# Optimization experiments

Measured on AMD Instinct MI355X. Metric: run time of the kernel, lower is better.

## Reference

```python
import jax, jax.numpy as jnp
import numpy as np

WIN = 12     # SAMv3 window_size
HEADS = 8    # num_heads

def _window(t, win=WIN):
    B, H, W, C = t.shape
    t = t.reshape(B, H // win, win, W // win, win, C).transpose(0, 1, 3, 2, 4, 5)
    return t.reshape(B, (H // win) * (W // win), win * win, C)

def _unwindow(t, H, W, win=WIN):
    B, nW, S, C = t.shape
    t = t.reshape(B, H // win, W // win, win, win, C).transpose(0, 1, 3, 2, 4, 5)
    return t.reshape(B, H, W, C)

def _sam(fq, fkv, bias, wq, wk, wv, wo, bo):
    # Windowed, masked cross-frame multi-head attention (SAMv3).
    # fq, fkv: (B, C, H, W); bias: (B, nW, 1, 1, S) additive mask bias.
    B, C, H, W = fq.shape
    hd = C // HEADS
    scale = hd ** -0.5
    q = _window(jnp.einsum('bchw,cd->bhwd', fq, wq))   # (B,nW,S,C)
    k = _window(jnp.einsum('bchw,cd->bhwd', fkv, wk))
    v = _window(jnp.einsum('bchw,cd->bhwd', fkv, wv))
    nW, S = q.shape[1], q.shape[2]
    q = q.reshape(B, nW, S, HEADS, hd)
    k = k.reshape(B, nW, S, HEADS, hd)
    v = v.reshape(B, nW, S, HEADS, hd)
    attn = jnp.einsum('bnqhd,bnkhd->bnhqk', q, k) * scale + bias
    attn = jax.nn.softmax(attn, axis=-1)
    out = jnp.einsum('bnhqk,bnkhd->bnqhd', attn, v).reshape(B, nW, S, C)
    out = out @ wo + bo
    return _unwindow(out, H, W).transpose(0, 3, 1, 2)  # (B, C, H, W)

def setup_inputs() -> dict:
    key = jax.random.key(0)
    B, C, T, H, W = 2, 384, 2, 192, 192
    ks = jax.random.split(key, 16)
    d = {}
    d['x'] = jax.random.normal(ks[0], (B, C, T, H, W), jnp.float32)
    d['mask'] = jax.random.randint(ks[1], (B, T, 1, H, W), 0, 2, jnp.int32)
    names = ['sam1_wq', 'sam1_wk', 'sam1_wv', 'sam1_wo',
             'sam2_wq', 'sam2_wk', 'sam2_wv', 'sam2_wo',
             'proj1_w', 'proj2_w']
    for i, n in enumerate(names):
        d[n] = jax.random.normal(ks[2 + i], (C, C), jnp.float32) * 0.02
    d['sam1_bo'] = jnp.zeros((C,), jnp.float32)
    d['sam2_bo'] = jnp.zeros((C,), jnp.float32)
    d['proj1_b'] = jnp.zeros((C,), jnp.float32)
    d['proj2_b'] = jnp.zeros((C,), jnp.float32)
    return d

def reference(x, mask, sam1_wq, sam1_wk, sam1_wv, sam1_wo, sam1_bo,
              sam2_wq, sam2_wk, sam2_wv, sam2_wo, sam2_bo,
              proj1_w, proj1_b, proj2_w, proj2_b):
    # x: (B, C, T=2, H, W); mask: (B, T, 1, H, W)
    f1 = x[:, :, 0]
    f2 = x[:, :, 1]
    m = mask[:, 1, 0][..., None]                      # (B, H, W, 1), frame-2 mask
    mw = _window(m)[..., 0]                           # (B, nW, S)
    bias = jnp.where(mw == 0, -1e9, 0.0).astype(x.dtype)[:, :, None, None, :]
    o1 = _sam(f1, f2, bias, sam1_wq, sam1_wk, sam1_wv, sam1_wo, sam1_bo)
    x1 = jnp.einsum('bchw,dc->bdhw', o1, proj1_w) + proj1_b[None, :, None, None]
    o2 = _sam(f2, f1, bias, sam2_wq, sam2_wk, sam2_wv, sam2_wo, sam2_bo)
    x2 = jnp.einsum('bchw,dc->bdhw', o2, proj2_w) + proj2_b[None, :, None, None]
    return jnp.concatenate([x1[:, :, None], x2[:, :, None]], axis=2)  # (B, C, 2, H, W)
```

## Files before the change

kernel.cpp:

```cpp
#include <hip/hip_runtime.h>
#include <stdint.h>

typedef __attribute__((ext_vector_type(8))) short bf16x8;
typedef __attribute__((ext_vector_type(4))) float f32x4;

#define HW    36864
#define CCH   384
#define NPIX  73728
#define W2    147456

__device__ __forceinline__ unsigned short f2bf(float f) {
  unsigned u = __builtin_bit_cast(unsigned, f);
  u += 0x7FFFu + ((u >> 16) & 1u);
  return (unsigned short)(u >> 16);
}

typedef const unsigned int __attribute__((address_space(1)))* gas1_t;
typedef unsigned int __attribute__((address_space(3)))* las3_t;
__device__ __forceinline__ void gload16(const void* g, void* l) {
  __builtin_amdgcn_global_load_lds((gas1_t)g, (las3_t)l, 16, 0, 0);
}


__global__ void k_wt(const float* __restrict__ w0, const float* __restrict__ w1,
                     const float* __restrict__ w2, const float* __restrict__ w3,
                     const float* __restrict__ w4, const float* __restrict__ w5,
                     unsigned short* __restrict__ wt) {
  int idx = blockIdx.x * 256 + threadIdx.x;
  int w = blockIdx.y;
  const float* W;
  switch (w) { case 0: W = w0; break; case 1: W = w1; break;
               case 2: W = w2; break; case 3: W = w3; break;
               case 4: W = w4; break; default: W = w5; break; }
  const int slotmap[6] = {0, 4, 5, 3, 1, 2};
  int slot = slotmap[w];
  int c = idx / 384, d = idx % 384;
  wt[(size_t)slot * W2 + (size_t)d * 384 + c] = f2bf(W[(size_t)c * 384 + d]);
}

__global__ void k_wf(const float* __restrict__ wo1, const float* __restrict__ pj1,
                     const float* __restrict__ wo2, const float* __restrict__ pj2,
                     unsigned short* __restrict__ wfT) {
  int idx = blockIdx.x * 256 + threadIdx.x;
  int s = blockIdx.y;
  const float* wo = s ? wo2 : wo1;
  const float* pj = s ? pj2 : pj1;
  int d = idx / 384, e = idx % 384;
  float acc = 0.f;
  for (int c = 0; c < 384; ++c) acc += pj[d * 384 + c] * wo[e * 384 + c];
  wfT[(size_t)s * W2 + (size_t)d * 384 + e] = f2bf(acc);
}

__global__ void k_bf(const float* __restrict__ bo1, const float* __restrict__ pj1,
                     const float* __restrict__ pb1, const float* __restrict__ bo2,
                     const float* __restrict__ pj2, const float* __restrict__ pb2,
                     float* __restrict__ bfused) {
  int t = threadIdx.x;
  int s = t / 384, d = t % 384;
  const float* bo = s ? bo2 : bo1;
  const float* pj = s ? pj2 : pj1;
  const float* pb = s ? pb2 : pb1;
  float acc = pb[d];
  for (int c = 0; c < 384; ++c) acc += pj[d * 384 + c] * bo[c];
  bfused[t] = acc;
}

__global__ __launch_bounds__(256) void k_tx(const float* __restrict__ x,
                                            unsigned short* __restrict__ xbf) {
  __shared__ float tile[64][65];
  int p0 = blockIdx.x * 64;
  int c0 = blockIdx.y * 64;
  int bt = blockIdx.z;
  int b = bt >> 1, t = bt & 1;
  int tid = threadIdx.x;
  int cl = tid >> 2;
  int pq = (tid & 3) * 4;
  const float* src = x + (((size_t)b * CCH + (c0 + cl)) * 2 + t) * HW + p0;
#pragma unroll
  for (int i = 0; i < 4; ++i) {
    int p_l = pq + i * 16;
    float4 v = *reinterpret_cast<const float4*>(src + p_l);
    tile[cl][p_l + 0] = v.x; tile[cl][p_l + 1] = v.y;
    tile[cl][p_l + 2] = v.z; tile[cl][p_l + 3] = v.w;
  }
  __syncthreads();
  int pl = tid >> 2;
  int cq = (tid & 3) * 16;
  unsigned short* dst = xbf + ((size_t)(t * 2 + b) * HW + p0 + pl) * CCH + c0 + cq;
  bf16x8 o0, o1;
#pragma unroll
  for (int j = 0; j < 8; ++j) o0[j] = (short)f2bf(tile[cq + j][pl]);
#pragma unroll
  for (int j = 0; j < 8; ++j) o1[j] = (short)f2bf(tile[cq + 8 + j][pl]);
  *reinterpret_cast<bf16x8*>(dst) = o0;
  *reinterpret_cast<bf16x8*>(dst + 8) = o1;
}

__global__ __launch_bounds__(256) void gemm_qkv(
    const unsigned short* __restrict__ A,
    const unsigned short* __restrict__ Bt,
    unsigned short* __restrict__ Cq,
    unsigned short* __restrict__ Ckv,
    float oscale) {
  __shared__ __align__(16) unsigned short Lsh[3][8192];
  const int tid = threadIdx.x;
  const int lane = tid & 63;
  const int wid = tid >> 6, wr = wid >> 1, wc = wid & 1;

  const int gx = gridDim.x;
  const int nwg = gx * gridDim.y;
  const int bid = blockIdx.x + blockIdx.y * gx;
  const int chunk = nwg >> 3;
  const int l = (bid & 7) * chunk + (bid >> 3);
  const int bx = l % gx, by = l / gx;

  const int m0 = by * 128;
  const int n0 = bx * 128;
  const int r15 = lane & 15, g = lane >> 4;

  const int u1 = tid + 256;
  const unsigned short* srcA0 = A + (size_t)(m0 + (tid >> 2)) * 384 + (((tid & 3) ^ ((tid >> 3) & 3)) << 3);
  const unsigned short* srcA1 = A + (size_t)(m0 + (u1 >> 2)) * 384 + (((u1 & 3) ^ ((u1 >> 3) & 3)) << 3);
  const unsigned short* srcB0 = Bt + (size_t)(n0 + (tid >> 2)) * 384 + (((tid & 3) ^ ((tid >> 3) & 3)) << 3);
  const unsigned short* srcB1 = Bt + (size_t)(n0 + (u1 >> 2)) * 384 + (((u1 & 3) ^ ((u1 >> 3) & 3)) << 3);
  const int wbase = (tid & ~63) * 8;

  f32x4 acc[4][4];
  f32x4 zero4 = {0.f, 0.f, 0.f, 0.f};
#pragma unroll
  for (int a = 0; a < 4; ++a)
#pragma unroll
    for (int b = 0; b < 4; ++b) acc[a][b] = zero4;

  const int swzr = (g ^ ((r15 >> 1) & 3)) << 3;

#define STAGE(buf, kt) do {                                  \
    int ke = (kt) * 32;                                      \
    gload16(srcA0 + ke, &Lsh[(buf)][wbase]);                 \
    gload16(srcA1 + ke, &Lsh[(buf)][2048 + wbase]);          \
    gload16(srcB0 + ke, &Lsh[(buf)][4096 + wbase]);          \
    gload16(srcB1 + ke, &Lsh[(buf)][6144 + wbase]);          \
  } while (0)

#define COMPUTE(buf) do {                                                       \
    bf16x8 af[4], bfv[4];                                                       \
    _Pragma("unroll")                                                           \
    for (int a = 0; a < 4; ++a)                                                 \
      af[a] = *(const bf16x8*)&Lsh[(buf)][(wr * 64 + a * 16 + r15) * 32 + swzr];\
    _Pragma("unroll")                                                           \
    for (int b = 0; b < 4; ++b)                                                 \
      bfv[b] = *(const bf16x8*)&Lsh[(buf)][4096 + (wc * 64 + b * 16 + r15) * 32 + swzr];\
    _Pragma("unroll")                                                           \
    for (int a = 0; a < 4; ++a)                                                 \
      _Pragma("unroll")                                                         \
      for (int b = 0; b < 4; ++b)                                               \
        acc[a][b] = __builtin_amdgcn_mfma_f32_16x16x32_bf16(af[a], bfv[b], acc[a][b], 0, 0, 0);\
  } while (0)

  STAGE(0, 0);
  STAGE(1, 1);
#pragma unroll
  for (int kt = 0; kt < 11; ++kt) {
    asm volatile("s_waitcnt vmcnt(4)" ::: "memory");
    __builtin_amdgcn_s_barrier();
    asm volatile("" ::: "memory");
    if (kt < 10) STAGE((kt + 2) % 3, kt + 2);
    COMPUTE(kt % 3);
  }
  __syncthreads();
  COMPUTE(11 % 3);
#undef STAGE
#undef COMPUTE

  unsigned short* Cp;
  int ldc2, ncol0;
  float sc;
  if (n0 < 384) { Cp = Cq;  ldc2 = 384; ncol0 = n0;       sc = oscale; }
  else          { Cp = Ckv; ldc2 = 768; ncol0 = n0 - 384; sc = 1.0f;   }
#pragma unroll
  for (int a = 0; a < 4; ++a) {
    size_t rbase = (size_t)(m0 + wr * 64 + a * 16 + g * 4) * ldc2;
#pragma unroll
    for (int b = 0; b < 4; ++b) {
      int n = ncol0 + wc * 64 + b * 16 + r15;
      unsigned short* cp = Cp + rbase + n;
#pragma unroll
      for (int r = 0; r < 4; ++r) cp[(size_t)r * ldc2] = f2bf(acc[a][b][r] * sc);
    }
  }
}

#define OPAD 408
__global__ __launch_bounds__(512, 2) void attn_kernel(
    const unsigned short* __restrict__ q,
    const unsigned short* __restrict__ kv,
    const int* __restrict__ mask,
    const unsigned short* __restrict__ wfT,
    const float* __restrict__ bfu,
    float* __restrict__ out,
    int tsel) {
  __shared__ __align__(16) unsigned short P[8][16][168];
  __shared__ __align__(16) unsigned short O_lds[144 * OPAD];
  __shared__ int ptab[144];
  const int n = blockIdx.x, b = blockIdx.y;
  const int tid = threadIdx.x;
  const int h = tid >> 6, lane = tid & 63;
  const int c15 = lane & 15, g = lane >> 4;
  const int wy = n >> 4, wx = n & 15;
  const size_t rowbase = (size_t)b * HW;
  const int* mrow = mask + (size_t)(b * 2 + 1) * HW;

  if (tid < 144)
    ptab[tid] = (wy * 12 + tid / 12) * 192 + wx * 12 + tid % 12;

  for (int idx = lane; idx < 16 * 24; idx += 64)
    P[h][idx / 24][144 + (idx % 24)] = 0;
  __syncthreads();

  float biasv[9];
#pragma unroll
  for (int nt = 0; nt < 9; ++nt)
    biasv[nt] = (mrow[ptab[nt * 16 + c15]] == 0) ? -1e9f : 0.0f;

  bf16x8 zfrag = {0, 0, 0, 0, 0, 0, 0, 0};
  f32x4 zero4 = {0.f, 0.f, 0.f, 0.f};

  bf16x8 kf0[9], kf1[9];
#pragma unroll
  for (int nt = 0; nt < 9; ++nt) {
    const unsigned short* kp = kv + (rowbase + ptab[nt * 16 + c15]) * 768 + h * 48;
    kf0[nt] = *(const bf16x8*)(kp + g * 8);
    kf1[nt] = zfrag;
    if (g < 2) kf1[nt] = *(const bf16x8*)(kp + 32 + g * 8);
  }

  const unsigned short* vb = kv + rowbase * 768 + 384 + h * 48;
  bf16x8 vf[5][3];
#pragma unroll
  for (int ks = 0; ks < 5; ++ks) {
#pragma unroll
    for (int dt = 0; dt < 3; ++dt) {
      bf16x8 v = {0, 0, 0, 0, 0, 0, 0, 0};
#pragma unroll
      for (int j = 0; j < 8; ++j) {
        int sk = ks * 32 + g * 8 + j;
        if (sk < 144)
          v[j] = (short)vb[(size_t)ptab[sk] * 768 + dt * 16 + c15];
      }
      vf[ks][dt] = v;
    }
  }

  bf16x8 qf0, qf1;
  {
    const unsigned short* qp = q + (rowbase + ptab[c15]) * 384 + h * 48;
    qf0 = *(const bf16x8*)(qp + g * 8);
    qf1 = zfrag;
    if (g < 2) qf1 = *(const bf16x8*)(qp + 32 + g * 8);
  }

  for (int mt = 0; mt < 9; ++mt) {
    bf16x8 qn0 = zfrag, qn1 = zfrag;
    if (mt < 8) {
      const unsigned short* qp = q + (rowbase + ptab[(mt + 1) * 16 + c15]) * 384 + h * 48;
      qn0 = *(const bf16x8*)(qp + g * 8);
      if (g < 2) qn1 = *(const bf16x8*)(qp + 32 + g * 8);
    }

    float l4[4] = {0.f, 0.f, 0.f, 0.f};
    f32x4 oacc[3];
#pragma unroll
    for (int dt = 0; dt < 3; ++dt) oacc[dt] = zero4;

#pragma unroll
    for (int nt = 0; nt < 9; ++nt) {
      f32x4 s = __builtin_amdgcn_mfma_f32_16x16x32_bf16(qf1, kf1[nt], zero4, 0, 0, 0);
      s = __builtin_amdgcn_mfma_f32_16x16x32_bf16(qf0, kf0[nt], s, 0, 0, 0);
#pragma unroll
      for (int r = 0; r < 4; ++r) {
        float pv = __expf(s[r] + biasv[nt]);
        l4[r] += pv;
        P[h][g * 4 + r][nt * 16 + c15] = f2bf(pv);
      }
      if (nt & 1) {
        int ks = nt >> 1;
        bf16x8 pf = *(const bf16x8*)&P[h][c15][ks * 32 + g * 8];
#pragma unroll
        for (int dt = 0; dt < 3; ++dt)
          oacc[dt] = __builtin_amdgcn_mfma_f32_16x16x32_bf16(pf, vf[ks][dt], oacc[dt], 0, 0, 0);
      }
    }
    {
      bf16x8 pf = *(const bf16x8*)&P[h][c15][4 * 32 + g * 8];
#pragma unroll
      for (int dt = 0; dt < 3; ++dt)
        oacc[dt] = __builtin_amdgcn_mfma_f32_16x16x32_bf16(pf, vf[4][dt], oacc[dt], 0, 0, 0);
    }

#pragma unroll
    for (int s = 1; s < 16; s <<= 1)
#pragma unroll
      for (int r = 0; r < 4; ++r) l4[r] += __shfl_xor(l4[r], s, 64);

    float inv[4];
#pragma unroll
    for (int r = 0; r < 4; ++r) inv[r] = 1.0f / l4[r];
#pragma unroll
    for (int dt = 0; dt < 3; ++dt) {
#pragma unroll
      for (int r = 0; r < 4; ++r) {
        int so = mt * 16 + g * 4 + r;
        O_lds[so * OPAD + h * 48 + dt * 16 + c15] = f2bf(oacc[dt][r] * inv[r]);
      }
    }

    qf0 = qn0; qf1 = qn1;
  }

  __syncthreads();

  {
    const unsigned short* wrow = wfT + (size_t)(h * 48) * 384;
    bf16x8 af[3][12];
#pragma unroll
    for (int mt2 = 0; mt2 < 3; ++mt2)
#pragma unroll
      for (int kt = 0; kt < 12; ++kt)
        af[mt2][kt] = *(const bf16x8*)(wrow + (size_t)(mt2 * 16 + c15) * 384 + kt * 32 + g * 8);

    float bias12[3][4];
#pragma unroll
    for (int mt2 = 0; mt2 < 3; ++mt2)
#pragma unroll
      for (int r = 0; r < 4; ++r)
        bias12[mt2][r] = bfu[h * 48 + mt2 * 16 + g * 4 + r];

#pragma unroll
    for (int ct = 0; ct < 9; ++ct) {
      bf16x8 bfr[12];
#pragma unroll
      for (int kt = 0; kt < 12; ++kt)
        bfr[kt] = *(const bf16x8*)&O_lds[(ct * 16 + c15) * OPAD + kt * 32 + g * 8];
      int pcol = ptab[ct * 16 + c15];
#pragma unroll
      for (int mt2 = 0; mt2 < 3; ++mt2) {
        f32x4 acc = zero4;
#pragma unroll
        for (int kt = 0; kt < 12; ++kt)
          acc = __builtin_amdgcn_mfma_f32_16x16x32_bf16(af[mt2][kt], bfr[kt], acc, 0, 0, 0);
#pragma unroll
        for (int r = 0; r < 4; ++r) {
          int d = h * 48 + mt2 * 16 + g * 4 + r;
          out[((size_t)(b * CCH + d) * 2 + tsel) * HW + pcol] = acc[r] + bias12[mt2][r];
        }
      }
    }
  }
}

extern "C" void kernel_launch(void* const* d_in, const int* in_sizes, int n_in,
                              void* d_out, int out_size, void* d_ws, size_t ws_size,
                              hipStream_t stream) {
  const float* x    = (const float*)d_in[0];
  const int*   mask = (const int*)d_in[1];
  const float* wq1 = (const float*)d_in[2];
  const float* wk1 = (const float*)d_in[3];
  const float* wv1 = (const float*)d_in[4];
  const float* wo1 = (const float*)d_in[5];
  const float* wq2 = (const float*)d_in[6];
  const float* wk2 = (const float*)d_in[7];
  const float* wv2 = (const float*)d_in[8];
  const float* wo2 = (const float*)d_in[9];
  const float* pj1 = (const float*)d_in[10];
  const float* pj2 = (const float*)d_in[11];
  const float* bo1 = (const float*)d_in[12];
  const float* bo2 = (const float*)d_in[13];
  const float* pb1 = (const float*)d_in[14];
  const float* pb2 = (const float*)d_in[15];
  float* out = (float*)d_out;

  const float SCALE = 0.14433756729740643f;

  char* ws = (char*)d_ws;
  size_t off = 0;
  unsigned short* wt   = (unsigned short*)(ws + off); off += (size_t)6 * W2 * 2;
  unsigned short* wfT  = (unsigned short*)(ws + off); off += (size_t)2 * W2 * 2;
  float*          bfu  = (float*)(ws + off);          off += (size_t)2 * 384 * 4;
  unsigned short* xbf  = (unsigned short*)(ws + off); off += (size_t)4 * HW * CCH * 2;
  size_t qsz = (size_t)NPIX * 384 * 2, kvsz = (size_t)NPIX * 768 * 2;
  unsigned short* qb0  = (unsigned short*)(ws + off); off += qsz;
  unsigned short* qb1  = (unsigned short*)(ws + off); off += qsz;
  unsigned short* kvb0 = (unsigned short*)(ws + off); off += kvsz;
  unsigned short* kvb1 = (unsigned short*)(ws + off); off += kvsz;
  if (ws_size < off) return;
  unsigned short* qb[2]  = {qb0, qb1};
  unsigned short* kvb[2] = {kvb0, kvb1};

  k_wt<<<dim3(576, 6), 256, 0, stream>>>(wq1, wk1, wv1, wq2, wk2, wv2, wt);
  k_wf<<<dim3(576, 2), 256, 0, stream>>>(wo1, pj1, wo2, pj2, wfT);
  k_bf<<<1, 768, 0, stream>>>(bo1, pj1, pb1, bo2, pj2, pb2, bfu);
  k_tx<<<dim3(576, 6, 4), 256, 0, stream>>>(x, xbf);

  for (int f = 0; f < 2; ++f) {
    gemm_qkv<<<dim3(9, 576), 256, 0, stream>>>(
        xbf + (size_t)f * 2 * HW * CCH, wt + (size_t)f * 3 * W2,
        qb[f], kvb[1 - f], SCALE);
  }
  for (int s = 0; s < 2; ++s) {
    attn_kernel<<<dim3(256, 2), 512, 0, stream>>>(
        qb[s], kvb[s], mask, wfT + (size_t)s * W2, bfu + s * 384, out, s);
  }
}
```

Measured before the change: 743.6 us.

## Unfuse output projection from attention and retile QKV GEMM to 256x128

Moves the fused output-projection GEMM out of the attention kernel into a separate gemm_out kernel. Attention now writes bf16 head outputs to a global buffer, which frees the large O_lds shared array and should raise attention occupancy. The QKV GEMM moves to 512-thread blocks with 256x128 tiles, a 64-wide K step, an 8-way XOR swizzle and s_setprio around the MFMAs. The cost is an extra global round trip of the attention output and two more kernel launches.

Measured after the change: 680.9 us. 1.09x faster.

```diff
diff --git a/kernel.cpp b/kernel.cpp
--- a/kernel.cpp
+++ b/kernel.cpp
@@ -96,16 +96,18 @@
   *reinterpret_cast<bf16x8*>(dst + 8) = o1;
 }
 
-__global__ __launch_bounds__(256) void gemm_qkv(
+__global__ __launch_bounds__(512) void gemm_qkv(
     const unsigned short* __restrict__ A,
     const unsigned short* __restrict__ Bt,
     unsigned short* __restrict__ Cq,
     unsigned short* __restrict__ Ckv,
     float oscale) {
-  __shared__ __align__(16) unsigned short Lsh[3][8192];
+  __shared__ __align__(16) unsigned short Lsh[3][24576];
   const int tid = threadIdx.x;
   const int lane = tid & 63;
-  const int wid = tid >> 6, wr = wid >> 1, wc = wid & 1;
+  const int wid = tid >> 6;
+  const int wr = wid >> 1, wc = wid & 1;
+  const int r15 = lane & 15, g = lane >> 4;
 
   const int gx = gridDim.x;
   const int nwg = gx * gridDim.y;
@@ -113,9 +115,115 @@
   const int chunk = nwg >> 3;
   const int l = (bid & 7) * chunk + (bid >> 3);
   const int bx = l % gx, by = l / gx;
-
-  const int m0 = by * 128;
-  const int n0 = bx * 128;
+  const int m0 = by * 256, n0 = bx * 128;
+
+  const int gsl = (tid & 7) ^ ((tid >> 3) & 7);
+  const unsigned short* srcA = A + (size_t)(m0 + (tid >> 3)) * 384 + gsl * 8;
+  const unsigned short* srcB = Bt + (size_t)(n0 + (tid >> 3)) * 384 + gsl * 8;
+  const int wu = tid & ~63;
+
+  f32x4 acc[4][4];
+  f32x4 zero4 = {0.f, 0.f, 0.f, 0.f};
+#pragma unroll
+  for (int a = 0; a < 4; ++a)
+#pragma unroll
+    for (int b = 0; b < 4; ++b) acc[a][b] = zero4;
+
+#define STAGE_A01(buf, kt) do {                                        \
+    size_t ko = (size_t)(kt) * 64;                                     \
+    gload16(srcA + ko,            &Lsh[(buf)][(wu) * 8]);              \
+    gload16(srcA + 64*384 + ko,   &Lsh[(buf)][(512 + wu) * 8]);        \
+    gload16(srcB + ko,            &Lsh[(buf)][16384 + (wu) * 8]);      \
+  } while (0)
+#define STAGE_A23(buf, kt) do {                                        \
+    size_t ko = (size_t)(kt) * 64;                                     \
+    gload16(srcA + 128*384 + ko,  &Lsh[(buf)][(1024 + wu) * 8]);       \
+    gload16(srcA + 192*384 + ko,  &Lsh[(buf)][(1536 + wu) * 8]);       \
+    gload16(srcB + 64*384 + ko,   &Lsh[(buf)][16384 + (512 + wu) * 8]);\
+  } while (0)
+
+  const int rsw = r15 & 7;
+
+#define PHASE(buf, ks) do {                                                     \
+    bf16x8 af[4], bfv[4];                                                       \
+    _Pragma("unroll")                                                           \
+    for (int a = 0; a < 4; ++a) {                                               \
+      int row = wr * 64 + a * 16 + r15;                                         \
+      af[a] = *(const bf16x8*)&Lsh[(buf)][row * 64 + (((ks)*4 + g) ^ rsw) * 8]; \
+    }                                                                           \
+    _Pragma("unroll")                                                           \
+    for (int b = 0; b < 4; ++b) {                                               \
+      int row = wc * 64 + b * 16 + r15;                                         \
+      bfv[b] = *(const bf16x8*)&Lsh[(buf)][16384 + row * 64 + (((ks)*4 + g) ^ rsw) * 8];\
+    }                                                                           \
+    __builtin_amdgcn_s_setprio(1);                                              \
+    _Pragma("unroll")                                                           \
+    for (int a = 0; a < 4; ++a)                                                 \
+      _Pragma("unroll")                                                         \
+      for (int b = 0; b < 4; ++b)                                               \
+        acc[a][b] = __builtin_amdgcn_mfma_f32_16x16x32_bf16(af[a], bfv[b], acc[a][b], 0, 0, 0);\
+    __builtin_amdgcn_s_setprio(0);                                              \
+  } while (0)
+
+  STAGE_A01(0, 0); STAGE_A23(0, 0);
+  STAGE_A01(1, 1); STAGE_A23(1, 1);
+
+#pragma unroll
+  for (int t = 0; t < 5; ++t) {
+    asm volatile("s_waitcnt vmcnt(6)" ::: "memory");
+    __builtin_amdgcn_s_barrier();
+    asm volatile("" ::: "memory");
+    const int buf = t % 3;
+    if (t < 4) STAGE_A01((t + 2) % 3, t + 2);
+    PHASE(buf, 0);
+    if (t < 4) STAGE_A23((t + 2) % 3, t + 2);
+    PHASE(buf, 1);
+  }
+  __syncthreads();
+  PHASE(2, 0);
+  PHASE(2, 1);
+#undef STAGE_A01
+#undef STAGE_A23
+#undef PHASE
+
+  unsigned short* Cp;
+  int ldc2, ncol0;
+  float sc;
+  if (n0 < 384) { Cp = Cq;  ldc2 = 384; ncol0 = n0;       sc = oscale; }
+  else          { Cp = Ckv; ldc2 = 768; ncol0 = n0 - 384; sc = 1.0f;   }
+#pragma unroll
+  for (int a = 0; a < 4; ++a) {
+    size_t rbase = (size_t)(m0 + wr * 64 + a * 16 + g * 4) * ldc2;
+#pragma unroll
+    for (int b = 0; b < 4; ++b) {
+      int n = ncol0 + wc * 64 + b * 16 + r15;
+      unsigned short* cp = Cp + rbase + n;
+#pragma unroll
+      for (int r = 0; r < 4; ++r) cp[(size_t)r * ldc2] = f2bf(acc[a][b][r] * sc);
+    }
+  }
+}
+
+__global__ __launch_bounds__(256) void gemm_out(
+    const unsigned short* __restrict__ A,
+    const unsigned short* __restrict__ Bt,
+    float* __restrict__ Cf,
+    const float* __restrict__ bias,
+    int tsel) {
+  __shared__ __align__(16) unsigned short Lsh[3][8192];
+  const int tid = threadIdx.x;
+  const int lane = tid & 63;
+  const int wid = tid >> 6, wr = wid >> 1, wc = wid & 1;
+
+  const int gx = gridDim.x;
+  const int nwg = gx * gridDim.y;
+  const int bid = blockIdx.x + blockIdx.y * gx;
+  const int chunk = nwg >> 3;
+  const int l = (bid & 7) * chunk + (bid >> 3);
+  const int bx = l % gx, by = l / gx;
+
+  const int m0 = bx * 128;
+  const int n0 = by * 128;
   const int r15 = lane & 15, g = lane >> 4;
 
   const int u1 = tid + 256;
@@ -172,35 +280,29 @@
 #undef STAGE
 #undef COMPUTE
 
-  unsigned short* Cp;
-  int ldc2, ncol0;
-  float sc;
-  if (n0 < 384) { Cp = Cq;  ldc2 = 384; ncol0 = n0;       sc = oscale; }
-  else          { Cp = Ckv; ldc2 = 768; ncol0 = n0 - 384; sc = 1.0f;   }
+  int bb = n0 / HW;
 #pragma unroll
   for (int a = 0; a < 4; ++a) {
-    size_t rbase = (size_t)(m0 + wr * 64 + a * 16 + g * 4) * ldc2;
+    int d = m0 + wr * 64 + a * 16 + g * 4;
 #pragma unroll
     for (int b = 0; b < 4; ++b) {
-      int n = ncol0 + wc * 64 + b * 16 + r15;
-      unsigned short* cp = Cp + rbase + n;
-#pragma unroll
-      for (int r = 0; r < 4; ++r) cp[(size_t)r * ldc2] = f2bf(acc[a][b][r] * sc);
-    }
-  }
-}
-
-#define OPAD 408
+      int n = n0 + wc * 64 + b * 16 + r15;
+      int p = n - bb * HW;
+#pragma unroll
+      for (int r = 0; r < 4; ++r) {
+        float v = acc[a][b][r] + bias[d + r];
+        Cf[(((size_t)bb * CCH + (d + r)) * 2 + tsel) * HW + p] = v;
+      }
+    }
+  }
+}
+
 __global__ __launch_bounds__(512, 2) void attn_kernel(
     const unsigned short* __restrict__ q,
     const unsigned short* __restrict__ kv,
     const int* __restrict__ mask,
-    const unsigned short* __restrict__ wfT,
-    const float* __restrict__ bfu,
-    float* __restrict__ out,
-    int tsel) {
+    unsigned short* __restrict__ obuf) {
   __shared__ __align__(16) unsigned short P[8][16][168];
-  __shared__ __align__(16) unsigned short O_lds[144 * OPAD];
   __shared__ int ptab[144];
   const int n = blockIdx.x, b = blockIdx.y;
   const int tid = threadIdx.x;
@@ -310,51 +412,12 @@
 #pragma unroll
       for (int r = 0; r < 4; ++r) {
         int so = mt * 16 + g * 4 + r;
-        O_lds[so * OPAD + h * 48 + dt * 16 + c15] = f2bf(oacc[dt][r] * inv[r]);
+        obuf[(rowbase + ptab[so]) * 384 + h * 48 + dt * 16 + c15] =
+            f2bf(oacc[dt][r] * inv[r]);
       }
     }
 
     qf0 = qn0; qf1 = qn1;
-  }
-
-  __syncthreads();
-
-  {
-    const unsigned short* wrow = wfT + (size_t)(h * 48) * 384;
-    bf16x8 af[3][12];
-#pragma unroll
-    for (int mt2 = 0; mt2 < 3; ++mt2)
-#pragma unroll
-      for (int kt = 0; kt < 12; ++kt)
-        af[mt2][kt] = *(const bf16x8*)(wrow + (size_t)(mt2 * 16 + c15) * 384 + kt * 32 + g * 8);
-
-    float bias12[3][4];
-#pragma unroll
-    for (int mt2 = 0; mt2 < 3; ++mt2)
-#pragma unroll
-      for (int r = 0; r < 4; ++r)
-        bias12[mt2][r] = bfu[h * 48 + mt2 * 16 + g * 4 + r];
-
-#pragma unroll
-    for (int ct = 0; ct < 9; ++ct) {
-      bf16x8 bfr[12];
-#pragma unroll
-      for (int kt = 0; kt < 12; ++kt)
-        bfr[kt] = *(const bf16x8*)&O_lds[(ct * 16 + c15) * OPAD + kt * 32 + g * 8];
-      int pcol = ptab[ct * 16 + c15];
-#pragma unroll
-      for (int mt2 = 0; mt2 < 3; ++mt2) {
-        f32x4 acc = zero4;
-#pragma unroll
-        for (int kt = 0; kt < 12; ++kt)
-          acc = __builtin_amdgcn_mfma_f32_16x16x32_bf16(af[mt2][kt], bfr[kt], acc, 0, 0, 0);
-#pragma unroll
-        for (int r = 0; r < 4; ++r) {
-          int d = h * 48 + mt2 * 16 + g * 4 + r;
-          out[((size_t)(b * CCH + d) * 2 + tsel) * HW + pcol] = acc[r] + bias12[mt2][r];
-        }
-      }
-    }
   }
 }
 
@@ -392,6 +455,7 @@
   unsigned short* qb1  = (unsigned short*)(ws + off); off += qsz;
   unsigned short* kvb0 = (unsigned short*)(ws + off); off += kvsz;
   unsigned short* kvb1 = (unsigned short*)(ws + off); off += kvsz;
+  unsigned short* obuf = (unsigned short*)(ws + off); off += qsz;
   if (ws_size < off) return;
   unsigned short* qb[2]  = {qb0, qb1};
   unsigned short* kvb[2] = {kvb0, kvb1};
@@ -402,12 +466,13 @@
   k_tx<<<dim3(576, 6, 4), 256, 0, stream>>>(x, xbf);
 
   for (int f = 0; f < 2; ++f) {
-    gemm_qkv<<<dim3(9, 576), 256, 0, stream>>>(
+    gemm_qkv<<<dim3(9, 288), 512, 0, stream>>>(
         xbf + (size_t)f * 2 * HW * CCH, wt + (size_t)f * 3 * W2,
         qb[f], kvb[1 - f], SCALE);
   }
   for (int s = 0; s < 2; ++s) {
-    attn_kernel<<<dim3(256, 2), 512, 0, stream>>>(
-        qb[s], kvb[s], mask, wfT + (size_t)s * W2, bfu + s * 384, out, s);
-  }
-}
+    attn_kernel<<<dim3(256, 2), 512, 0, stream>>>(qb[s], kvb[s], mask, obuf);
+    gemm_out<<<dim3(3, 576), 256, 0, stream>>>(
+        wfT + (size_t)s * W2, obuf, out, bfu + s * 384, s);
+  }
+}
```
